# Performance work log

Measured on AMD Instinct MI355X. Metric: run time of the kernel, lower is better.

The kernel has to match this reference:

```python
import jax, jax.numpy as jnp
import numpy as np

B, S, H = 64, 512, 768
NUM_BD = 5
N_CLASSES = 9
N_REGIONS = 4096
GAMMA = 0.3


def setup_inputs() -> dict:
    key = jax.random.key(0)
    ks = jax.random.split(key, 11)
    return {
        "word_repr": jax.random.normal(ks[0], (B, S, H), dtype=jnp.float32),
        "W_s": jax.random.normal(ks[1], (H, NUM_BD), dtype=jnp.float32) * 0.02,
        "b_s": jax.random.normal(ks[2], (NUM_BD,), dtype=jnp.float32) * 0.02,
        "W_r": jax.random.normal(ks[3], (H, N_CLASSES), dtype=jnp.float32) * 0.02,
        "b_r": jax.random.normal(ks[4], (N_CLASSES,), dtype=jnp.float32) * 0.02,
        "bd_tgt": jax.random.randint(ks[5], (B, S), 0, NUM_BD),
        "seg": jax.random.randint(ks[6], (B, S), 0, 2),
        "region_starts": jax.random.randint(ks[7], (N_REGIONS,), 0, 495),
        "region_lengths": jax.random.randint(ks[8], (N_REGIONS,), 0, 16),
        "region_batch": jax.random.randint(ks[9], (N_REGIONS,), 0, B),
        "region_labels": jax.random.randint(ks[10], (N_REGIONS,), 0, N_CLASSES),
    }


def reference(word_repr, W_s, b_s, W_r, b_r, bd_tgt, seg,
              region_starts, region_lengths, region_batch, region_labels):
    dt = word_repr.dtype
    b, s, h = word_repr.shape

    # sentence boundary logits [B,S,5]
    sent_out = jnp.einsum('bsh,hk->bsk', word_repr, W_s) + b_s

    # --- region mean pooling via exclusive prefix sums (fused segment-mean) ---
    cs = jnp.concatenate(
        [jnp.zeros((b, 1, h), dt), jnp.cumsum(word_repr, axis=1)], axis=1)  # [B,S+1,H]
    ends = region_starts + region_lengths  # inclusive end index
    seg_sum = cs[region_batch, ends + 1] - cs[region_batch, region_starts]  # [R,H]
    lens = (region_lengths + 1).astype(dt)
    region_repr = seg_sum / lens[:, None]

    # region classification + cross-entropy (mean)
    region_logits = region_repr @ W_r + b_r  # [R,C]
    logp_r = jax.nn.log_softmax(region_logits, axis=-1)
    ent_loss = -jnp.mean(
        jnp.take_along_axis(logp_r, region_labels[:, None], axis=1)[:, 0])

    # boundary loss: masked mean NLL with one-hot targets
    logp_s = jax.nn.log_softmax(sent_out.reshape(-1, NUM_BD), axis=-1)
    nll = -jnp.take_along_axis(logp_s, bd_tgt.reshape(-1, 1), axis=1)[:, 0]
    mask = seg.reshape(-1).astype(dt)
    bd_loss = jnp.sum(mask * nll) / (jnp.sum(mask) + 1e-6)

    return GAMMA * ent_loss + (1.0 - GAMMA) * bd_loss
```

## Files before the change

### kernel.cpp

```cpp
#include <hip/hip_runtime.h>

#define BB 64
#define SS 512
#define HH 768
#define HH4 (HH / 4)
#define NBD 5
#define NC 9
#define NR 4096
#define NTOK (BB * SS)

__global__ __launch_bounds__(256) void bd_kernel(
    const float* __restrict__ wr, const float* __restrict__ Ws,
    const float* __restrict__ bs, const int* __restrict__ tgt,
    const int* __restrict__ seg, float2* __restrict__ out_part)
{
    const int wid  = threadIdx.x >> 6;
    const int lane = threadIdx.x & 63;
    const int gw   = blockIdx.x * 4 + wid;

    float wreg[3][4][NBD];
    #pragma unroll
    for (int j = 0; j < 3; ++j) {
        const float4* wp = (const float4*)(Ws + (4 * lane + 256 * j) * NBD);
        #pragma unroll
        for (int p = 0; p < 5; ++p) {
            const float4 f = wp[p];
            const float vv[4] = {f.x, f.y, f.z, f.w};
            #pragma unroll
            for (int q = 0; q < 4; ++q) {
                const int flat = 4 * p + q;
                wreg[j][flat / NBD][flat % NBD] = vv[q];
            }
        }
    }
    const float b0 = bs[0], b1 = bs[1], b2 = bs[2], b3 = bs[3], b4 = bs[4];

    const float4* base = (const float4*)wr + (size_t)(4 * gw) * HH4;
    float4 v[4][3];
    #pragma unroll
    for (int i = 0; i < 4; ++i)
        #pragma unroll
        for (int j = 0; j < 3; ++j)
            v[i][j] = base[i * HH4 + lane + 64 * j];

    float nll_sum = 0.f, msk_sum = 0.f;

    #pragma unroll
    for (int i = 0; i < 4; ++i) {
        float dot[NBD] = {0.f, 0.f, 0.f, 0.f, 0.f};
        #pragma unroll
        for (int j = 0; j < 3; ++j) {
            const float x[4] = {v[i][j].x, v[i][j].y, v[i][j].z, v[i][j].w};
            #pragma unroll
            for (int e = 0; e < 4; ++e)
                #pragma unroll
                for (int k = 0; k < NBD; ++k)
                    dot[k] += x[e] * wreg[j][e][k];
        }

        #pragma unroll
        for (int k = 0; k < NBD; ++k)
            #pragma unroll
            for (int off = 32; off; off >>= 1)
                dot[k] += __shfl_xor(dot[k], off);

        if (lane == 0) {
            const int token = 4 * gw + i;
            float l[NBD] = {dot[0] + b0, dot[1] + b1, dot[2] + b2,
                            dot[3] + b3, dot[4] + b4};
            float m = l[0];
            #pragma unroll
            for (int k = 1; k < NBD; ++k) m = fmaxf(m, l[k]);
            float ssum = 0.f;
            #pragma unroll
            for (int k = 0; k < NBD; ++k) ssum += expf(l[k] - m);
            const float lse = logf(ssum);
            const int   t   = tgt[token];
            const float msk = (float)seg[token];
            nll_sum += msk * (-(l[t] - m - lse));
            msk_sum += msk;
        }
    }

    __shared__ float s_n[4], s_m[4];
    if (lane == 0) { s_n[wid] = nll_sum; s_m[wid] = msk_sum; }
    __syncthreads();
    if (threadIdx.x == 0) {
        out_part[blockIdx.x] =
            make_float2(s_n[0] + s_n[1] + s_n[2] + s_n[3],
                        s_m[0] + s_m[1] + s_m[2] + s_m[3]);
    }
}

__global__ __launch_bounds__(256) void region_kernel(
    const float* __restrict__ wr, const float* __restrict__ Wr,
    const float* __restrict__ br, const int* __restrict__ rstart,
    const int* __restrict__ rlen, const int* __restrict__ rbatch,
    const int* __restrict__ rlabel, float* __restrict__ out_nll)
{
    const int wid  = threadIdx.x >> 6;
    const int lane = threadIdx.x & 63;
    const int r    = blockIdx.x * 4 + wid;

    const int   start = rstart[r];
    const int   len   = rlen[r] + 1;
    const int   b     = rbatch[r];
    const float inv   = 1.0f / (float)len;

    const float4* base =
        (const float4*)wr + ((size_t)b * SS + start) * HH4;

    float4 m0 = {0.f, 0.f, 0.f, 0.f};
    float4 m1 = {0.f, 0.f, 0.f, 0.f};
    float4 m2 = {0.f, 0.f, 0.f, 0.f};

    #pragma unroll
    for (int row = 0; row < 16; ++row) {
        const int rc = (row < len) ? row : (len - 1);
        const float4 u0 = base[(size_t)rc * HH4 + lane];
        const float4 u1 = base[(size_t)rc * HH4 + lane + 64];
        const float4 u2 = base[(size_t)rc * HH4 + lane + 128];
        const float  w  = (row < len) ? inv : 0.f;
        m0.x += w * u0.x; m0.y += w * u0.y; m0.z += w * u0.z; m0.w += w * u0.w;
        m1.x += w * u1.x; m1.y += w * u1.y; m1.z += w * u1.z; m1.w += w * u1.w;
        m2.x += w * u2.x; m2.y += w * u2.y; m2.z += w * u2.z; m2.w += w * u2.w;
    }

    float part[NC];
    #pragma unroll
    for (int c = 0; c < NC; ++c) part[c] = 0.f;

    const float mv[3][4] = {{m0.x, m0.y, m0.z, m0.w},
                            {m1.x, m1.y, m1.z, m1.w},
                            {m2.x, m2.y, m2.z, m2.w}};
    #pragma unroll
    for (int g = 0; g < 3; ++g) {
        const int f = lane + 64 * g;
        const float4* wv = (const float4*)(Wr + (size_t)4 * f * NC);
        #pragma unroll
        for (int j = 0; j < 9; ++j) {
            const float4 x = wv[j];
            const float vv[4] = {x.x, x.y, x.z, x.w};
            #pragma unroll
            for (int q = 0; q < 4; ++q) {
                const int flat = 4 * j + q;
                part[flat % NC] += mv[g][flat / NC] * vv[q];
            }
        }
    }

    #pragma unroll
    for (int c = 0; c < NC; ++c)
        #pragma unroll
        for (int off = 32; off; off >>= 1)
            part[c] += __shfl_xor(part[c], off);

    if (lane == 0) {
        float l[NC];
        #pragma unroll
        for (int c = 0; c < NC; ++c) l[c] = part[c] + br[c];
        float mx = l[0];
        #pragma unroll
        for (int c = 1; c < NC; ++c) mx = fmaxf(mx, l[c]);
        float ssum = 0.f;
        #pragma unroll
        for (int c = 0; c < NC; ++c) ssum += expf(l[c] - mx);
        const float lse = logf(ssum);
        const int   t   = rlabel[r];
        out_nll[r] = -(l[t] - mx - lse);
    }
}

__global__ __launch_bounds__(256) void fin_kernel(
    const float2* __restrict__ bdp, const float* __restrict__ rnll,
    float* __restrict__ out)
{
    const int tid  = threadIdx.x;
    const int wid  = tid >> 6;
    const int lane = tid & 63;

    double a = 0.0, c = 0.0, e = 0.0;
    for (int i = tid; i < 2048; i += 256) {
        const float2 p = bdp[i];
        a += (double)p.x;
        c += (double)p.y;
    }
    for (int i = tid; i < NR; i += 256) e += (double)rnll[i];

    #pragma unroll
    for (int off = 32; off; off >>= 1) {
        a += __shfl_xor(a, off);
        c += __shfl_xor(c, off);
        e += __shfl_xor(e, off);
    }

    __shared__ double sa[4], sc[4], se[4];
    if (lane == 0) { sa[wid] = a; sc[wid] = c; se[wid] = e; }
    __syncthreads();

    if (tid == 0) {
        const double A = sa[0] + sa[1] + sa[2] + sa[3];
        const double C = sc[0] + sc[1] + sc[2] + sc[3];
        const double E = se[0] + se[1] + se[2] + se[3];
        const float ent = (float)(E / (double)NR);
        const float bd  = (float)(A / (C + 1e-6));
        out[0] = 0.3f * ent + 0.7f * bd;
    }
}

extern "C" void kernel_launch(void* const* d_in, const int* in_sizes, int n_in,
                              void* d_out, int out_size, void* d_ws, size_t ws_size,
                              hipStream_t stream)
{
    const float* wr     = (const float*)d_in[0];
    const float* Ws     = (const float*)d_in[1];
    const float* bs     = (const float*)d_in[2];
    const float* Wr     = (const float*)d_in[3];
    const float* br     = (const float*)d_in[4];
    const int*   tgt    = (const int*)d_in[5];
    const int*   seg    = (const int*)d_in[6];
    const int*   rstart = (const int*)d_in[7];
    const int*   rlen   = (const int*)d_in[8];
    const int*   rbatch = (const int*)d_in[9];
    const int*   rlabel = (const int*)d_in[10];

    float2* bdp  = (float2*)d_ws;
    float*  rnll = (float*)((char*)d_ws + 2048 * sizeof(float2));

    region_kernel<<<NR / 4, 256, 0, stream>>>(wr, Wr, br, rstart, rlen,
                                              rbatch, rlabel, rnll);
    bd_kernel<<<NTOK / 16, 256, 0, stream>>>(wr, Ws, bs, tgt, seg, bdp);
    fin_kernel<<<1, 256, 0, stream>>>(bdp, rnll, (float*)d_out);
}
```

Baseline: 195.3 us.

## Fuse region, boundary and final reduction kernels into one launch with last-block finish

New measurement: 428.9 us. 2.2x slower.

```diff
diff --git a/kernel.cpp b/kernel.cpp
--- a/kernel.cpp
+++ b/kernel.cpp
@@ -7,181 +7,186 @@
 #define NBD 5
 #define NC 9
 #define NR 4096
-#define NTOK (BB * SS)
-
-__global__ __launch_bounds__(256) void bd_kernel(
+#define NB_BD 2048
+#define NB_RG 1024
+#define NBLK (NB_BD + NB_RG)
+
+__global__ __launch_bounds__(256) void fused_kernel(
     const float* __restrict__ wr, const float* __restrict__ Ws,
     const float* __restrict__ bs, const int* __restrict__ tgt,
-    const int* __restrict__ seg, float2* __restrict__ out_part)
-{
-    const int wid  = threadIdx.x >> 6;
-    const int lane = threadIdx.x & 63;
-    const int gw   = blockIdx.x * 4 + wid;
-
-    float wreg[3][4][NBD];
-    #pragma unroll
-    for (int j = 0; j < 3; ++j) {
-        const float4* wp = (const float4*)(Ws + (4 * lane + 256 * j) * NBD);
-        #pragma unroll
-        for (int p = 0; p < 5; ++p) {
-            const float4 f = wp[p];
-            const float vv[4] = {f.x, f.y, f.z, f.w};
-            #pragma unroll
-            for (int q = 0; q < 4; ++q) {
-                const int flat = 4 * p + q;
-                wreg[j][flat / NBD][flat % NBD] = vv[q];
-            }
-        }
-    }
-    const float b0 = bs[0], b1 = bs[1], b2 = bs[2], b3 = bs[3], b4 = bs[4];
-
-    const float4* base = (const float4*)wr + (size_t)(4 * gw) * HH4;
-    float4 v[4][3];
-    #pragma unroll
-    for (int i = 0; i < 4; ++i)
-        #pragma unroll
-        for (int j = 0; j < 3; ++j)
-            v[i][j] = base[i * HH4 + lane + 64 * j];
-
-    float nll_sum = 0.f, msk_sum = 0.f;
-
-    #pragma unroll
-    for (int i = 0; i < 4; ++i) {
-        float dot[NBD] = {0.f, 0.f, 0.f, 0.f, 0.f};
-        #pragma unroll
-        for (int j = 0; j < 3; ++j) {
-            const float x[4] = {v[i][j].x, v[i][j].y, v[i][j].z, v[i][j].w};
-            #pragma unroll
-            for (int e = 0; e < 4; ++e)
-                #pragma unroll
-                for (int k = 0; k < NBD; ++k)
-                    dot[k] += x[e] * wreg[j][e][k];
-        }
-
-        #pragma unroll
-        for (int k = 0; k < NBD; ++k)
-            #pragma unroll
-            for (int off = 32; off; off >>= 1)
-                dot[k] += __shfl_xor(dot[k], off);
-
-        if (lane == 0) {
-            const int token = 4 * gw + i;
-            float l[NBD] = {dot[0] + b0, dot[1] + b1, dot[2] + b2,
-                            dot[3] + b3, dot[4] + b4};
-            float m = l[0];
-            #pragma unroll
-            for (int k = 1; k < NBD; ++k) m = fmaxf(m, l[k]);
-            float ssum = 0.f;
-            #pragma unroll
-            for (int k = 0; k < NBD; ++k) ssum += expf(l[k] - m);
-            const float lse = logf(ssum);
-            const int   t   = tgt[token];
-            const float msk = (float)seg[token];
-            nll_sum += msk * (-(l[t] - m - lse));
-            msk_sum += msk;
-        }
-    }
-
-    __shared__ float s_n[4], s_m[4];
-    if (lane == 0) { s_n[wid] = nll_sum; s_m[wid] = msk_sum; }
-    __syncthreads();
-    if (threadIdx.x == 0) {
-        out_part[blockIdx.x] =
-            make_float2(s_n[0] + s_n[1] + s_n[2] + s_n[3],
-                        s_m[0] + s_m[1] + s_m[2] + s_m[3]);
-    }
-}
-
-__global__ __launch_bounds__(256) void region_kernel(
-    const float* __restrict__ wr, const float* __restrict__ Wr,
-    const float* __restrict__ br, const int* __restrict__ rstart,
-    const int* __restrict__ rlen, const int* __restrict__ rbatch,
-    const int* __restrict__ rlabel, float* __restrict__ out_nll)
-{
-    const int wid  = threadIdx.x >> 6;
-    const int lane = threadIdx.x & 63;
-    const int r    = blockIdx.x * 4 + wid;
-
-    const int   start = rstart[r];
-    const int   len   = rlen[r] + 1;
-    const int   b     = rbatch[r];
-    const float inv   = 1.0f / (float)len;
-
-    const float4* base =
-        (const float4*)wr + ((size_t)b * SS + start) * HH4;
-
-    float4 m0 = {0.f, 0.f, 0.f, 0.f};
-    float4 m1 = {0.f, 0.f, 0.f, 0.f};
-    float4 m2 = {0.f, 0.f, 0.f, 0.f};
-
-    #pragma unroll
-    for (int row = 0; row < 16; ++row) {
-        const int rc = (row < len) ? row : (len - 1);
-        const float4 u0 = base[(size_t)rc * HH4 + lane];
-        const float4 u1 = base[(size_t)rc * HH4 + lane + 64];
-        const float4 u2 = base[(size_t)rc * HH4 + lane + 128];
-        const float  w  = (row < len) ? inv : 0.f;
-        m0.x += w * u0.x; m0.y += w * u0.y; m0.z += w * u0.z; m0.w += w * u0.w;
-        m1.x += w * u1.x; m1.y += w * u1.y; m1.z += w * u1.z; m1.w += w * u1.w;
-        m2.x += w * u2.x; m2.y += w * u2.y; m2.z += w * u2.z; m2.w += w * u2.w;
-    }
-
-    float part[NC];
-    #pragma unroll
-    for (int c = 0; c < NC; ++c) part[c] = 0.f;
-
-    const float mv[3][4] = {{m0.x, m0.y, m0.z, m0.w},
-                            {m1.x, m1.y, m1.z, m1.w},
-                            {m2.x, m2.y, m2.z, m2.w}};
-    #pragma unroll
-    for (int g = 0; g < 3; ++g) {
-        const int f = lane + 64 * g;
-        const float4* wv = (const float4*)(Wr + (size_t)4 * f * NC);
-        #pragma unroll
-        for (int j = 0; j < 9; ++j) {
-            const float4 x = wv[j];
-            const float vv[4] = {x.x, x.y, x.z, x.w};
-            #pragma unroll
-            for (int q = 0; q < 4; ++q) {
-                const int flat = 4 * j + q;
-                part[flat % NC] += mv[g][flat / NC] * vv[q];
-            }
-        }
-    }
-
-    #pragma unroll
-    for (int c = 0; c < NC; ++c)
-        #pragma unroll
-        for (int off = 32; off; off >>= 1)
-            part[c] += __shfl_xor(part[c], off);
-
-    if (lane == 0) {
-        float l[NC];
-        #pragma unroll
-        for (int c = 0; c < NC; ++c) l[c] = part[c] + br[c];
-        float mx = l[0];
-        #pragma unroll
-        for (int c = 1; c < NC; ++c) mx = fmaxf(mx, l[c]);
-        float ssum = 0.f;
-        #pragma unroll
-        for (int c = 0; c < NC; ++c) ssum += expf(l[c] - mx);
-        const float lse = logf(ssum);
-        const int   t   = rlabel[r];
-        out_nll[r] = -(l[t] - mx - lse);
-    }
-}
-
-__global__ __launch_bounds__(256) void fin_kernel(
-    const float2* __restrict__ bdp, const float* __restrict__ rnll,
-    float* __restrict__ out)
+    const int* __restrict__ seg,
+    const float* __restrict__ Wr, const float* __restrict__ br,
+    const int* __restrict__ rstart, const int* __restrict__ rlen,
+    const int* __restrict__ rbatch, const int* __restrict__ rlabel,
+    float2* __restrict__ bd_part, float* __restrict__ rnll,
+    unsigned int* __restrict__ counter, float* __restrict__ out)
 {
     const int tid  = threadIdx.x;
     const int wid  = tid >> 6;
     const int lane = tid & 63;
+    const int bid  = blockIdx.x;
+
+    if (bid % 3 != 0) {
+        const int bb = bid - bid / 3 - 1;
+        const int gw = bb * 4 + wid;
+
+        float wreg[3][4][NBD];
+        #pragma unroll
+        for (int j = 0; j < 3; ++j) {
+            const float4* wp = (const float4*)(Ws + (4 * lane + 256 * j) * NBD);
+            #pragma unroll
+            for (int p = 0; p < 5; ++p) {
+                const float4 f = wp[p];
+                const float vv[4] = {f.x, f.y, f.z, f.w};
+                #pragma unroll
+                for (int q = 0; q < 4; ++q) {
+                    const int flat = 4 * p + q;
+                    wreg[j][flat / NBD][flat % NBD] = vv[q];
+                }
+            }
+        }
+        const float b0 = bs[0], b1 = bs[1], b2 = bs[2], b3 = bs[3], b4 = bs[4];
+
+        const float4* base = (const float4*)wr + (size_t)(4 * gw) * HH4;
+        float4 v[4][3];
+        #pragma unroll
+        for (int i = 0; i < 4; ++i)
+            #pragma unroll
+            for (int j = 0; j < 3; ++j)
+                v[i][j] = base[i * HH4 + lane + 64 * j];
+
+        float nll_sum = 0.f, msk_sum = 0.f;
+
+        #pragma unroll
+        for (int i = 0; i < 4; ++i) {
+            float dot[NBD] = {0.f, 0.f, 0.f, 0.f, 0.f};
+            #pragma unroll
+            for (int j = 0; j < 3; ++j) {
+                const float x[4] = {v[i][j].x, v[i][j].y, v[i][j].z, v[i][j].w};
+                #pragma unroll
+                for (int e = 0; e < 4; ++e)
+                    #pragma unroll
+                    for (int k = 0; k < NBD; ++k)
+                        dot[k] += x[e] * wreg[j][e][k];
+            }
+
+            #pragma unroll
+            for (int k = 0; k < NBD; ++k)
+                #pragma unroll
+                for (int off = 32; off; off >>= 1)
+                    dot[k] += __shfl_xor(dot[k], off);
+
+            if (lane == 0) {
+                const int token = 4 * gw + i;
+                float l[NBD] = {dot[0] + b0, dot[1] + b1, dot[2] + b2,
+                                dot[3] + b3, dot[4] + b4};
+                float m = l[0];
+                #pragma unroll
+                for (int k = 1; k < NBD; ++k) m = fmaxf(m, l[k]);
+                float ssum = 0.f;
+                #pragma unroll
+                for (int k = 0; k < NBD; ++k) ssum += expf(l[k] - m);
+                const float lse = logf(ssum);
+                const int   t   = tgt[token];
+                const float msk = (float)seg[token];
+                nll_sum += msk * (-(l[t] - m - lse));
+                msk_sum += msk;
+            }
+        }
+
+        __shared__ float s_n[4], s_m[4];
+        if (lane == 0) { s_n[wid] = nll_sum; s_m[wid] = msk_sum; }
+        __syncthreads();
+        if (tid == 0) {
+            bd_part[bb] = make_float2(s_n[0] + s_n[1] + s_n[2] + s_n[3],
+                                      s_m[0] + s_m[1] + s_m[2] + s_m[3]);
+        }
+    } else {
+        const int r = (bid / 3) * 4 + wid;
+
+        const int   start = rstart[r];
+        const int   len   = rlen[r] + 1;
+        const int   b     = rbatch[r];
+        const float inv   = 1.0f / (float)len;
+
+        const float4* base =
+            (const float4*)wr + ((size_t)b * SS + start) * HH4;
+
+        float4 m0 = {0.f, 0.f, 0.f, 0.f};
+        float4 m1 = {0.f, 0.f, 0.f, 0.f};
+        float4 m2 = {0.f, 0.f, 0.f, 0.f};
+
+        #pragma unroll
+        for (int row = 0; row < 16; ++row) {
+            const int rc = (row < len) ? row : (len - 1);
+            const float4 u0 = base[(size_t)rc * HH4 + lane];
+            const float4 u1 = base[(size_t)rc * HH4 + lane + 64];
+            const float4 u2 = base[(size_t)rc * HH4 + lane + 128];
+            const float  w  = (row < len) ? inv : 0.f;
+            m0.x += w * u0.x; m0.y += w * u0.y; m0.z += w * u0.z; m0.w += w * u0.w;
+            m1.x += w * u1.x; m1.y += w * u1.y; m1.z += w * u1.z; m1.w += w * u1.w;
+            m2.x += w * u2.x; m2.y += w * u2.y; m2.z += w * u2.z; m2.w += w * u2.w;
+        }
+
+        float part[NC];
+        #pragma unroll
+        for (int c = 0; c < NC; ++c) part[c] = 0.f;
+
+        const float mv[3][4] = {{m0.x, m0.y, m0.z, m0.w},
+                                {m1.x, m1.y, m1.z, m1.w},
+                                {m2.x, m2.y, m2.z, m2.w}};
+        #pragma unroll
+        for (int g = 0; g < 3; ++g) {
+            const int f = lane + 64 * g;
+            const float4* wv = (const float4*)(Wr + (size_t)4 * f * NC);
+            #pragma unroll
+            for (int j = 0; j < 9; ++j) {
+                const float4 x = wv[j];
+                const float vv[4] = {x.x, x.y, x.z, x.w};
+                #pragma unroll
+                for (int q = 0; q < 4; ++q) {
+                    const int flat = 4 * j + q;
+                    part[flat % NC] += mv[g][flat / NC] * vv[q];
+                }
+            }
+        }
+
+        #pragma unroll
+        for (int c = 0; c < NC; ++c)
+            #pragma unroll
+            for (int off = 32; off; off >>= 1)
+                part[c] += __shfl_xor(part[c], off);
+
+        if (lane == 0) {
+            float l[NC];
+            #pragma unroll
+            for (int c = 0; c < NC; ++c) l[c] = part[c] + br[c];
+            float mx = l[0];
+            #pragma unroll
+            for (int c = 1; c < NC; ++c) mx = fmaxf(mx, l[c]);
+            float ssum = 0.f;
+            #pragma unroll
+            for (int c = 0; c < NC; ++c) ssum += expf(l[c] - mx);
+            const float lse = logf(ssum);
+            const int   t   = rlabel[r];
+            rnll[r] = -(l[t] - mx - lse);
+        }
+    }
+
+    __syncthreads();
+    __shared__ bool s_last;
+    if (tid == 0) {
+        __threadfence();
+        const unsigned int old = atomicAdd(counter, 1u);
+        s_last = (old == (unsigned int)(NBLK - 1));
+        __threadfence();
+    }
+    __syncthreads();
+    if (!s_last) return;
 
     double a = 0.0, c = 0.0, e = 0.0;
-    for (int i = tid; i < 2048; i += 256) {
-        const float2 p = bdp[i];
+    for (int i = tid; i < NB_BD; i += 256) {
+        const float2 p = bd_part[i];
         a += (double)p.x;
         c += (double)p.y;
     }
@@ -224,11 +229,13 @@
     const int*   rbatch = (const int*)d_in[9];
     const int*   rlabel = (const int*)d_in[10];
 
-    float2* bdp  = (float2*)d_ws;
-    float*  rnll = (float*)((char*)d_ws + 2048 * sizeof(float2));
-
-    region_kernel<<<NR / 4, 256, 0, stream>>>(wr, Wr, br, rstart, rlen,
-                                              rbatch, rlabel, rnll);
-    bd_kernel<<<NTOK / 16, 256, 0, stream>>>(wr, Ws, bs, tgt, seg, bdp);
-    fin_kernel<<<1, 256, 0, stream>>>(bdp, rnll, (float*)d_out);
+    float2*       bdp  = (float2*)d_ws;
+    float*        rnll = (float*)((char*)d_ws + NB_BD * sizeof(float2));
+    unsigned int* ctr  = (unsigned int*)((char*)d_ws + NB_BD * sizeof(float2)
+                                         + NR * sizeof(float));
+
+    hipMemsetAsync(ctr, 0, sizeof(unsigned int), stream);
+    fused_kernel<<<NBLK, 256, 0, stream>>>(wr, Ws, bs, tgt, seg,
+                                           Wr, br, rstart, rlen, rbatch, rlabel,
+                                           bdp, rnll, ctr, (float*)d_out);
 }
```
